# Performance work log

Measured on AMD Instinct MI355X. Metric: run time of the kernel, lower is better.

## Reference

```python
import jax, jax.numpy as jnp
import numpy as np

DIM = 256
NUM_HEADS = 8
HEAD_DIM = DIM // NUM_HEADS


def setup_inputs() -> dict:
    key = jax.random.key(0)
    k1, k2, k3, k4 = jax.random.split(key, 4)
    b, n = 4, 2048
    x = jax.random.normal(k1, (b, n, DIM), dtype=jnp.float32)
    # Linear weights with fan-in scaling (matches nn.Linear init magnitude,
    # keeps exp(qk) numerically sane since the original has no max-subtraction).
    Wqkv = jax.random.normal(k2, (DIM, 3 * DIM), dtype=jnp.float32) * (DIM ** -0.5)
    Wout = jax.random.normal(k3, (DIM, DIM), dtype=jnp.float32) * (DIM ** -0.5)
    bout = jax.random.normal(k4, (DIM,), dtype=jnp.float32) * 0.01
    return {"x": x, "Wqkv": Wqkv, "Wout": Wout, "bout": bout}


def reference(x, Wqkv, Wout, bout):
    b, n, d = x.shape
    h, hd = NUM_HEADS, HEAD_DIM
    scale = hd ** -0.5
    qkv = x @ Wqkv  # [b, n, 3d]
    q, k, v = jnp.split(qkv, 3, axis=-1)
    # [b, h, n, hd]
    q = q.reshape(b, n, h, hd).transpose(0, 2, 1, 3) * scale
    k = k.reshape(b, n, h, hd).transpose(0, 2, 1, 3)
    v = v.reshape(b, n, h, hd).transpose(0, 2, 1, 3)
    # Original KeOps path: unnormalized exp (no max-subtraction), separate
    # numerator / denominator reductions, eps in denominator.
    scores = jnp.einsum('bhnd,bhmd->bhnm', q, k)  # [b, h, n, n]
    e = jnp.exp(scores)
    denom = jnp.sum(e, axis=-1, keepdims=True)          # [b, h, n, 1]
    numer = jnp.einsum('bhnm,bhmd->bhnd', e, v)         # [b, h, n, hd]
    out = numer / (denom + 1e-6)
    out = out.transpose(0, 2, 1, 3).reshape(b, n, d)
    return out @ Wout + bout
```

## Files before the change

### kernel.cpp

```cpp
#include <hip/hip_runtime.h>

#define DIM 256
#define NHEADS 8
#define HDIM 32

typedef _Float16 half8_t __attribute__((ext_vector_type(8)));
typedef _Float16 half4_t __attribute__((ext_vector_type(4)));
typedef float float4_t __attribute__((ext_vector_type(4)));

__device__ __forceinline__ void gload_lds16(const void* g, void* l) {
    __builtin_amdgcn_global_load_lds((const __attribute__((address_space(1))) void*)g,
                                     (__attribute__((address_space(3))) void*)l,
                                     16, 0, 0);
}

__global__ __launch_bounds__(256) void prep(const float* __restrict__ x,
                                            const float* __restrict__ Wqkv,
                                            const float* __restrict__ Wout,
                                            _Float16* __restrict__ xh,
                                            _Float16* __restrict__ WqT,
                                            _Float16* __restrict__ WoT) {
    __shared__ float ts[32][33];
    const int bid = blockIdx.x, t = threadIdx.x;
    if (bid < 1024) {
        size_t idx = (size_t)bid * 2048 + (size_t)t * 8;
        float tmp[8];
        *reinterpret_cast<float4*>(tmp)     = *reinterpret_cast<const float4*>(x + idx);
        *reinterpret_cast<float4*>(tmp + 4) = *reinterpret_cast<const float4*>(x + idx + 4);
        half8_t h;
        #pragma unroll
        for (int j = 0; j < 8; ++j) h[j] = (_Float16)tmp[j];
        *reinterpret_cast<half8_t*>(xh + idx) = h;
    } else {
        const float* src; _Float16* dst; int K, N, kb, nb;
        if (bid < 1024 + 192) { int b2 = bid - 1024; src = Wqkv; dst = WqT; K = 256; N = 768; nb = b2 % 24; kb = b2 / 24; }
        else                  { int b3 = bid - 1216; src = Wout; dst = WoT; K = 256; N = 256; nb = b3 % 8;  kb = b3 / 8; }
        const int tx = t & 31, ty = t >> 5;
        #pragma unroll
        for (int i = 0; i < 4; ++i) {
            int k = kb * 32 + ty + i * 8;
            ts[ty + i * 8][tx] = src[(size_t)k * N + nb * 32 + tx];
        }
        __syncthreads();
        #pragma unroll
        for (int i = 0; i < 4; ++i) {
            int nl = ty + i * 8;
            dst[(size_t)(nb * 32 + nl) * K + kb * 32 + tx] = (_Float16)ts[tx][nl];
        }
    }
}

__global__ __launch_bounds__(256) void gemm_qkv(const _Float16* __restrict__ A,
                                                const _Float16* __restrict__ BT,
                                                _Float16* __restrict__ qh,
                                                _Float16* __restrict__ kpack,
                                                _Float16* __restrict__ vp) {
    __shared__ alignas(16) _Float16 As[64 * 32];
    __shared__ alignas(16) _Float16 Bs[128 * 32];
    const int t = threadIdx.x, lane = t & 63, wave = t >> 6;
    const int l16 = lane & 15, quad = lane >> 4;
    const int m0 = blockIdx.y * 64, n0 = blockIdx.x * 128;
    const int wr = (wave >> 1) * 32, wc = (wave & 1) * 64;
    const int K = 256;

    float4_t acc[2][4];
    #pragma unroll
    for (int i = 0; i < 2; ++i)
        #pragma unroll
        for (int j = 0; j < 4; ++j) acc[i][j] = (float4_t){0.f, 0.f, 0.f, 0.f};

    const int srow = lane >> 2;
    const int scol = (lane & 3) * 8;

    for (int k0 = 0; k0 < K; k0 += 32) {
        gload_lds16(A  + (size_t)(m0 + wave * 16 + srow) * K + k0 + scol, As + wave * 512);
        gload_lds16(BT + (size_t)(n0 + wave * 16 + srow) * K + k0 + scol, Bs + wave * 512);
        gload_lds16(BT + (size_t)(n0 + 64 + wave * 16 + srow) * K + k0 + scol, Bs + 2048 + wave * 512);
        __syncthreads();
        half8_t af[2], bf[4];
        #pragma unroll
        for (int i = 0; i < 2; ++i)
            af[i] = *reinterpret_cast<const half8_t*>(As + (wr + i * 16 + l16) * 32 + quad * 8);
        #pragma unroll
        for (int j = 0; j < 4; ++j)
            bf[j] = *reinterpret_cast<const half8_t*>(Bs + (wc + j * 16 + l16) * 32 + quad * 8);
        #pragma unroll
        for (int i = 0; i < 2; ++i)
            #pragma unroll
            for (int j = 0; j < 4; ++j)
                acc[i][j] = __builtin_amdgcn_mfma_f32_16x16x32_f16(af[i], bf[j], acc[i][j], 0, 0, 0);
        __syncthreads();
    }

    const int bb = m0 >> 11;
    if (n0 < 256) {
        #pragma unroll
        for (int i = 0; i < 2; ++i)
            #pragma unroll
            for (int r = 0; r < 4; ++r) {
                int row = m0 + wr + i * 16 + quad * 4 + r;
                #pragma unroll
                for (int j = 0; j < 4; ++j)
                    qh[(size_t)row * 256 + n0 + wc + j * 16 + l16] = (_Float16)acc[i][j][r];
            }
    } else if (n0 < 512) {
        #pragma unroll
        for (int i = 0; i < 2; ++i)
            #pragma unroll
            for (int r = 0; r < 4; ++r) {
                int tok = (m0 & 2047) + wr + i * 16 + quad * 4 + r;
                #pragma unroll
                for (int j = 0; j < 4; ++j) {
                    int kc = n0 + wc + j * 16 + l16 - 256;
                    int hh = kc >> 5, dd = kc & 31;
                    kpack[((size_t)(bb * NHEADS + hh) * 2048 + tok) * 32 + dd] =
                        (_Float16)acc[i][j][r];
                }
            }
    } else {
        #pragma unroll
        for (int i = 0; i < 2; ++i) {
            int tok0 = (m0 & 2047) + wr + i * 16 + quad * 4;
            int chunk = tok0 >> 5, tl = tok0 & 31;
            #pragma unroll
            for (int j = 0; j < 4; ++j) {
                int vc = n0 + wc + j * 16 + l16 - 512;
                int hh = vc >> 5, dd = vc & 31;
                half4_t p;
                #pragma unroll
                for (int r = 0; r < 4; ++r) p[r] = (_Float16)acc[i][j][r];
                *reinterpret_cast<half4_t*>(
                    vp + (((size_t)(bb * NHEADS + hh) * 64 + chunk) * 32 + dd) * 32 + tl) = p;
            }
        }
    }
}

__global__ __launch_bounds__(256, 2) void attn_v7(const _Float16* __restrict__ qh,
                                                  const _Float16* __restrict__ kpack,
                                                  const _Float16* __restrict__ vp,
                                                  _Float16* __restrict__ NUM,
                                                  float* __restrict__ DEN) {
    __shared__ alignas(16) _Float16 es[4][64][40];
    const int bid = blockIdx.x;
    const int kh = bid & 1;
    const int qb = (bid >> 1) & 7;
    const int bh = bid >> 4;
    const int b = bh >> 3, h = bh & 7;
    const int t = threadIdx.x, lane = t & 63, wave = t >> 6;
    const int l16 = lane & 15, quad = lane >> 4;
    const float scale = 0.17677669529663687f;
    const int bN = b * 2048;
    const int q0w = qb * 256 + wave * 64;
    const int kbeg = kh * 1024;

    half8_t qf[4];
    {
        const _Float16* qrow = qh + (size_t)(bN + q0w + l16) * 256 + h * HDIM + quad * 8;
        #pragma unroll
        for (int g = 0; g < 4; ++g)
            qf[g] = *reinterpret_cast<const half8_t*>(qrow + (size_t)g * 16 * 256);
    }

    const _Float16* kb_ = kpack + (size_t)bh * 65536;
    const _Float16* vb_ = vp + (size_t)bh * 65536;

    float4_t num[4][2];
    #pragma unroll
    for (int g = 0; g < 4; ++g)
        #pragma unroll
        for (int dt = 0; dt < 2; ++dt) num[g][dt] = (float4_t){0.f, 0.f, 0.f, 0.f};
    float ds[4] = {0.f, 0.f, 0.f, 0.f};
    _Float16* esw = &es[wave][0][0];
    const float4_t z = {0.f, 0.f, 0.f, 0.f};

    for (int k0 = kbeg; k0 < kbeg + 1024; k0 += 64) {
        half8_t kf[4], vf[4];
        #pragma unroll
        for (int j = 0; j < 4; ++j)
            kf[j] = *reinterpret_cast<const half8_t*>(
                kb_ + (size_t)(k0 + j * 16 + l16) * 32 + quad * 8);
        const int c0 = k0 >> 5;
        #pragma unroll
        for (int s = 0; s < 2; ++s)
            #pragma unroll
            for (int m = 0; m < 2; ++m)
                vf[s * 2 + m] = *reinterpret_cast<const half8_t*>(
                    vb_ + ((size_t)(c0 + s) * 32 + m * 16 + l16) * 32 + quad * 8);

        float4_t st[4][4];
        #pragma unroll
        for (int kb = 0; kb < 4; ++kb)
            #pragma unroll
            for (int g = 0; g < 4; ++g)
                st[kb][g] = __builtin_amdgcn_mfma_f32_16x16x32_f16(kf[kb], qf[g], z, 0, 0, 0);

        half4_t ep[4][4];
        #pragma unroll
        for (int kb = 0; kb < 4; ++kb)
            #pragma unroll
            for (int g = 0; g < 4; ++g)
                #pragma unroll
                for (int r = 0; r < 4; ++r) {
                    float e = __expf(st[kb][g][r] * scale);
                    ds[g] += e;
                    ep[kb][g][r] = (_Float16)e;
                }

        #pragma unroll
        for (int s = 0; s < 2; ++s) {
            #pragma unroll
            for (int tt = 0; tt < 2; ++tt)
                #pragma unroll
                for (int g = 0; g < 4; ++g)
                    *reinterpret_cast<half4_t*>(
                        esw + (g * 16 + l16) * 40 + tt * 16 + quad * 4) = ep[s * 2 + tt][g];

            #pragma unroll
            for (int g = 0; g < 4; ++g) {
                half8_t ef = *reinterpret_cast<const half8_t*>(
                    esw + (g * 16 + l16) * 40 + quad * 8);
                num[g][0] = __builtin_amdgcn_mfma_f32_16x16x32_f16(ef, vf[s * 2],     num[g][0], 0, 0, 0);
                num[g][1] = __builtin_amdgcn_mfma_f32_16x16x32_f16(ef, vf[s * 2 + 1], num[g][1], 0, 0, 0);
            }
        }
    }

    #pragma unroll
    for (int g = 0; g < 4; ++g) {
        ds[g] += __shfl_xor(ds[g], 16, 64);
        ds[g] += __shfl_xor(ds[g], 32, 64);
    }

    _Float16* ob = NUM + (size_t)kh * 2097152 + (size_t)(bN + q0w) * DIM + h * HDIM;
    #pragma unroll
    for (int g = 0; g < 4; ++g)
        #pragma unroll
        for (int r = 0; r < 4; ++r) {
            size_t ro = (size_t)(g * 16 + quad * 4 + r) * DIM;
            ob[ro + l16]      = (_Float16)num[g][0][r];
            ob[ro + 16 + l16] = (_Float16)num[g][1][r];
        }
    if (quad == 0) {
        #pragma unroll
        for (int g = 0; g < 4; ++g)
            DEN[kh * 65536 + bh * 2048 + q0w + g * 16 + l16] = ds[g];
    }
}

__global__ __launch_bounds__(256) void gemm2c(const _Float16* __restrict__ NUM,
                                              const float* __restrict__ DEN,
                                              const _Float16* __restrict__ BT,
                                              const float* __restrict__ bias,
                                              float* __restrict__ out) {
    __shared__ alignas(16) _Float16 As[64 * 32];
    __shared__ alignas(16) _Float16 Bs[64 * 32];
    const int t = threadIdx.x, lane = t & 63, wave = t >> 6;
    const int l16 = lane & 15, quad = lane >> 4;
    const int m0 = blockIdx.y * 64, n0 = blockIdx.x * 64;
    const int wr = (wave >> 1) * 32, wc = (wave & 1) * 32;
    const int bb = m0 >> 11;

    const int arow = t >> 2;
    const int acol = (t & 3) * 8;
    const int myrow = m0 + arow;
    _Float16 rcp8[8];
    #pragma unroll
    for (int hh = 0; hh < 8; ++hh) {
        int di = (bb * 8 + hh) * 2048 + (myrow & 2047);
        rcp8[hh] = (_Float16)(1.f / (DEN[di] + DEN[di + 65536] + 1e-6f));
    }
    const _Float16* np = NUM + (size_t)myrow * 256 + acol;

    float4_t acc[2][2];
    #pragma unroll
    for (int i = 0; i < 2; ++i)
        #pragma unroll
        for (int j = 0; j < 2; ++j) acc[i][j] = (float4_t){0.f, 0.f, 0.f, 0.f};

    for (int k0 = 0; k0 < 256; k0 += 32) {
        half8_t n0h = *reinterpret_cast<const half8_t*>(np + k0);
        half8_t n1h = *reinterpret_cast<const half8_t*>(np + k0 + 2097152);
        *reinterpret_cast<half8_t*>(As + arow * 32 + acol) = (n0h + n1h) * rcp8[k0 >> 5];
        gload_lds16(BT + (size_t)(n0 + arow) * 256 + k0 + acol, Bs + t * 8);
        __syncthreads();
        half8_t af[2], bf[2];
        #pragma unroll
        for (int i = 0; i < 2; ++i)
            af[i] = *reinterpret_cast<const half8_t*>(As + (wr + i * 16 + l16) * 32 + quad * 8);
        #pragma unroll
        for (int j = 0; j < 2; ++j)
            bf[j] = *reinterpret_cast<const half8_t*>(Bs + (wc + j * 16 + l16) * 32 + quad * 8);
        #pragma unroll
        for (int i = 0; i < 2; ++i)
            #pragma unroll
            for (int j = 0; j < 2; ++j)
                acc[i][j] = __builtin_amdgcn_mfma_f32_16x16x32_f16(af[i], bf[j], acc[i][j], 0, 0, 0);
        __syncthreads();
    }

    #pragma unroll
    for (int i = 0; i < 2; ++i)
        #pragma unroll
        for (int r = 0; r < 4; ++r) {
            int row = m0 + wr + i * 16 + quad * 4 + r;
            #pragma unroll
            for (int j = 0; j < 2; ++j) {
                int col = n0 + wc + j * 16 + l16;
                out[(size_t)row * 256 + col] = acc[i][j][r] + bias[col];
            }
        }
}

extern "C" void kernel_launch(void* const* d_in, const int* in_sizes, int n_in,
                              void* d_out, int out_size, void* d_ws, size_t ws_size,
                              hipStream_t stream) {
    const float* x    = (const float*)d_in[0];
    const float* Wqkv = (const float*)d_in[1];
    const float* Wout = (const float*)d_in[2];
    const float* bout = (const float*)d_in[3];
    float* out = (float*)d_out;
    const int M = 8192;

    _Float16* xh    = (_Float16*)d_ws;
    _Float16* WqT   = xh + (size_t)M * DIM;
    _Float16* WoT   = WqT + 768 * 256;
    _Float16* qh    = WoT + 256 * 256;
    _Float16* kpack = qh + (size_t)M * DIM;
    _Float16* vp    = kpack + (size_t)32 * 2048 * 32;
    _Float16* NUM   = vp + (size_t)32 * 2048 * 32;
    float*    DEN   = (float*)(NUM + (size_t)2 * M * DIM);

    hipLaunchKernelGGL(prep, dim3(1280), dim3(256), 0, stream, x, Wqkv, Wout, xh, WqT, WoT);
    hipLaunchKernelGGL(gemm_qkv, dim3(6, 128), dim3(256), 0, stream, xh, WqT, qh, kpack, vp);
    hipLaunchKernelGGL(attn_v7, dim3(512), dim3(256), 0, stream, qh, kpack, vp, NUM, DEN);
    hipLaunchKernelGGL(gemm2c, dim3(4, 128), dim3(256), 0, stream, NUM, DEN, WoT, bout, out);
}
```

Before: 126.0 us.

## Split attention keys four ways, fold scale into Q, use MFMA for row sums

The x-to-fp16 conversion moves out of the prep kernel and into the QKV GEMM's A-tile load, so the xh round trip through memory goes away. The softmax scale times log2(e) is folded into Q at GEMM time so attention can use exp2 directly. The attention denominator is now accumulated with an extra MFMA against a ones vector, replacing the scalar adds and shuffles. The key range is split four ways instead of two, doubling the block count with launch bounds of 4, at the cost of more partial NUM/DEN traffic that the output GEMM must sum.

```diff
diff --git a/kernel.cpp b/kernel.cpp
--- a/kernel.cpp
+++ b/kernel.cpp
@@ -14,43 +14,30 @@
                                      16, 0, 0);
 }
 
-__global__ __launch_bounds__(256) void prep(const float* __restrict__ x,
-                                            const float* __restrict__ Wqkv,
-                                            const float* __restrict__ Wout,
-                                            _Float16* __restrict__ xh,
-                                            _Float16* __restrict__ WqT,
-                                            _Float16* __restrict__ WoT) {
+#define QSCALE 0.25503093964976485f
+
+__global__ __launch_bounds__(256) void prep_w(const float* __restrict__ Wqkv,
+                                              const float* __restrict__ Wout,
+                                              _Float16* __restrict__ WqT,
+                                              _Float16* __restrict__ WoT) {
     __shared__ float ts[32][33];
     const int bid = blockIdx.x, t = threadIdx.x;
-    if (bid < 1024) {
-        size_t idx = (size_t)bid * 2048 + (size_t)t * 8;
-        float tmp[8];
-        *reinterpret_cast<float4*>(tmp)     = *reinterpret_cast<const float4*>(x + idx);
-        *reinterpret_cast<float4*>(tmp + 4) = *reinterpret_cast<const float4*>(x + idx + 4);
-        half8_t h;
-        #pragma unroll
-        for (int j = 0; j < 8; ++j) h[j] = (_Float16)tmp[j];
-        *reinterpret_cast<half8_t*>(xh + idx) = h;
-    } else {
-        const float* src; _Float16* dst; int K, N, kb, nb;
-        if (bid < 1024 + 192) { int b2 = bid - 1024; src = Wqkv; dst = WqT; K = 256; N = 768; nb = b2 % 24; kb = b2 / 24; }
-        else                  { int b3 = bid - 1216; src = Wout; dst = WoT; K = 256; N = 256; nb = b3 % 8;  kb = b3 / 8; }
-        const int tx = t & 31, ty = t >> 5;
-        #pragma unroll
-        for (int i = 0; i < 4; ++i) {
-            int k = kb * 32 + ty + i * 8;
-            ts[ty + i * 8][tx] = src[(size_t)k * N + nb * 32 + tx];
-        }
-        __syncthreads();
-        #pragma unroll
-        for (int i = 0; i < 4; ++i) {
-            int nl = ty + i * 8;
-            dst[(size_t)(nb * 32 + nl) * K + kb * 32 + tx] = (_Float16)ts[tx][nl];
-        }
-    }
-}
-
-__global__ __launch_bounds__(256) void gemm_qkv(const _Float16* __restrict__ A,
+    const float* src; _Float16* dst; int N, kb, nb;
+    if (bid < 192) { src = Wqkv; dst = WqT; N = 768; nb = bid % 24; kb = bid / 24; }
+    else           { int b3 = bid - 192; src = Wout; dst = WoT; N = 256; nb = b3 % 8; kb = b3 / 8; }
+    const int tx = t & 31, ty = t >> 5;
+    #pragma unroll
+    for (int i = 0; i < 4; ++i)
+        ts[ty + i * 8][tx] = src[(size_t)(kb * 32 + ty + i * 8) * N + nb * 32 + tx];
+    __syncthreads();
+    #pragma unroll
+    for (int i = 0; i < 4; ++i) {
+        int nl = ty + i * 8;
+        dst[(size_t)(nb * 32 + nl) * 256 + kb * 32 + tx] = (_Float16)ts[tx][nl];
+    }
+}
+
+__global__ __launch_bounds__(256) void gemm_qkv(const float* __restrict__ x,
                                                 const _Float16* __restrict__ BT,
                                                 _Float16* __restrict__ qh,
                                                 _Float16* __restrict__ kpack,
@@ -69,11 +56,22 @@
         #pragma unroll
         for (int j = 0; j < 4; ++j) acc[i][j] = (float4_t){0.f, 0.f, 0.f, 0.f};
 
+    const int arow = t >> 2;
+    const int acol = (t & 3) * 8;
     const int srow = lane >> 2;
     const int scol = (lane & 3) * 8;
 
     for (int k0 = 0; k0 < K; k0 += 32) {
-        gload_lds16(A  + (size_t)(m0 + wave * 16 + srow) * K + k0 + scol, As + wave * 512);
+        {
+            const float* xp = x + (size_t)(m0 + arow) * K + k0 + acol;
+            float tmp[8];
+            *reinterpret_cast<float4*>(tmp)     = *reinterpret_cast<const float4*>(xp);
+            *reinterpret_cast<float4*>(tmp + 4) = *reinterpret_cast<const float4*>(xp + 4);
+            half8_t h;
+            #pragma unroll
+            for (int j = 0; j < 8; ++j) h[j] = (_Float16)tmp[j];
+            *reinterpret_cast<half8_t*>(As + arow * 32 + acol) = h;
+        }
         gload_lds16(BT + (size_t)(n0 + wave * 16 + srow) * K + k0 + scol, Bs + wave * 512);
         gload_lds16(BT + (size_t)(n0 + 64 + wave * 16 + srow) * K + k0 + scol, Bs + 2048 + wave * 512);
         __syncthreads();
@@ -101,7 +99,8 @@
                 int row = m0 + wr + i * 16 + quad * 4 + r;
                 #pragma unroll
                 for (int j = 0; j < 4; ++j)
-                    qh[(size_t)row * 256 + n0 + wc + j * 16 + l16] = (_Float16)acc[i][j][r];
+                    qh[(size_t)row * 256 + n0 + wc + j * 16 + l16] =
+                        (_Float16)(acc[i][j][r] * QSCALE);
             }
     } else if (n0 < 512) {
         #pragma unroll
@@ -136,23 +135,22 @@
     }
 }
 
-__global__ __launch_bounds__(256, 2) void attn_v7(const _Float16* __restrict__ qh,
+__global__ __launch_bounds__(256, 4) void attn_v8(const _Float16* __restrict__ qh,
                                                   const _Float16* __restrict__ kpack,
                                                   const _Float16* __restrict__ vp,
                                                   _Float16* __restrict__ NUM,
                                                   float* __restrict__ DEN) {
     __shared__ alignas(16) _Float16 es[4][64][40];
     const int bid = blockIdx.x;
-    const int kh = bid & 1;
-    const int qb = (bid >> 1) & 7;
-    const int bh = bid >> 4;
+    const int kh = bid & 3;
+    const int qb = (bid >> 2) & 7;
+    const int bh = bid >> 5;
     const int b = bh >> 3, h = bh & 7;
     const int t = threadIdx.x, lane = t & 63, wave = t >> 6;
     const int l16 = lane & 15, quad = lane >> 4;
-    const float scale = 0.17677669529663687f;
     const int bN = b * 2048;
     const int q0w = qb * 256 + wave * 64;
-    const int kbeg = kh * 1024;
+    const int kbeg = kh * 512;
 
     half8_t qf[4];
     {
@@ -165,16 +163,22 @@
     const _Float16* kb_ = kpack + (size_t)bh * 65536;
     const _Float16* vb_ = vp + (size_t)bh * 65536;
 
-    float4_t num[4][2];
-    #pragma unroll
-    for (int g = 0; g < 4; ++g)
-        #pragma unroll
-        for (int dt = 0; dt < 2; ++dt) num[g][dt] = (float4_t){0.f, 0.f, 0.f, 0.f};
-    float ds[4] = {0.f, 0.f, 0.f, 0.f};
+    float4_t num[4][2], dacc[4];
+    #pragma unroll
+    for (int g = 0; g < 4; ++g) {
+        num[g][0] = (float4_t){0.f, 0.f, 0.f, 0.f};
+        num[g][1] = (float4_t){0.f, 0.f, 0.f, 0.f};
+        dacc[g]   = (float4_t){0.f, 0.f, 0.f, 0.f};
+    }
+    half8_t ones;
+    #pragma unroll
+    for (int j = 0; j < 8; ++j) ones[j] = (_Float16)1.0f;
+
     _Float16* esw = &es[wave][0][0];
     const float4_t z = {0.f, 0.f, 0.f, 0.f};
 
-    for (int k0 = kbeg; k0 < kbeg + 1024; k0 += 64) {
+    #pragma unroll 2
+    for (int k0 = kbeg; k0 < kbeg + 512; k0 += 64) {
         half8_t kf[4], vf[4];
         #pragma unroll
         for (int j = 0; j < 4; ++j)
@@ -201,11 +205,8 @@
             #pragma unroll
             for (int g = 0; g < 4; ++g)
                 #pragma unroll
-                for (int r = 0; r < 4; ++r) {
-                    float e = __expf(st[kb][g][r] * scale);
-                    ds[g] += e;
-                    ep[kb][g][r] = (_Float16)e;
-                }
+                for (int r = 0; r < 4; ++r)
+                    ep[kb][g][r] = (_Float16)__builtin_exp2f(st[kb][g][r]);
 
         #pragma unroll
         for (int s = 0; s < 2; ++s) {
@@ -222,14 +223,9 @@
                     esw + (g * 16 + l16) * 40 + quad * 8);
                 num[g][0] = __builtin_amdgcn_mfma_f32_16x16x32_f16(ef, vf[s * 2],     num[g][0], 0, 0, 0);
                 num[g][1] = __builtin_amdgcn_mfma_f32_16x16x32_f16(ef, vf[s * 2 + 1], num[g][1], 0, 0, 0);
-            }
-        }
-    }
-
-    #pragma unroll
-    for (int g = 0; g < 4; ++g) {
-        ds[g] += __shfl_xor(ds[g], 16, 64);
-        ds[g] += __shfl_xor(ds[g], 32, 64);
+                dacc[g]   = __builtin_amdgcn_mfma_f32_16x16x32_f16(ef, ones,          dacc[g],   0, 0, 0);
+            }
+        }
     }
 
     _Float16* ob = NUM + (size_t)kh * 2097152 + (size_t)(bN + q0w) * DIM + h * HDIM;
@@ -241,10 +237,12 @@
             ob[ro + l16]      = (_Float16)num[g][0][r];
             ob[ro + 16 + l16] = (_Float16)num[g][1][r];
         }
-    if (quad == 0) {
+    if (l16 == 0) {
         #pragma unroll
         for (int g = 0; g < 4; ++g)
-            DEN[kh * 65536 + bh * 2048 + q0w + g * 16 + l16] = ds[g];
+            #pragma unroll
+            for (int r = 0; r < 4; ++r)
+                DEN[kh * 65536 + bh * 2048 + q0w + g * 16 + quad * 4 + r] = dacc[g][r];
     }
 }
 
@@ -268,7 +266,8 @@
     #pragma unroll
     for (int hh = 0; hh < 8; ++hh) {
         int di = (bb * 8 + hh) * 2048 + (myrow & 2047);
-        rcp8[hh] = (_Float16)(1.f / (DEN[di] + DEN[di + 65536] + 1e-6f));
+        float d = DEN[di] + DEN[di + 65536] + DEN[di + 131072] + DEN[di + 196608];
+        rcp8[hh] = (_Float16)(1.f / (d + 1e-6f));
     }
     const _Float16* np = NUM + (size_t)myrow * 256 + acol;
 
@@ -279,9 +278,12 @@
         for (int j = 0; j < 2; ++j) acc[i][j] = (float4_t){0.f, 0.f, 0.f, 0.f};
 
     for (int k0 = 0; k0 < 256; k0 += 32) {
-        half8_t n0h = *reinterpret_cast<const half8_t*>(np + k0);
-        half8_t n1h = *reinterpret_cast<const half8_t*>(np + k0 + 2097152);
-        *reinterpret_cast<half8_t*>(As + arow * 32 + acol) = (n0h + n1h) * rcp8[k0 >> 5];
+        half8_t s0 = *reinterpret_cast<const half8_t*>(np + k0);
+        half8_t s1 = *reinterpret_cast<const half8_t*>(np + k0 + 2097152);
+        half8_t s2 = *reinterpret_cast<const half8_t*>(np + k0 + 2 * 2097152);
+        half8_t s3 = *reinterpret_cast<const half8_t*>(np + k0 + 3 * 2097152);
+        *reinterpret_cast<half8_t*>(As + arow * 32 + acol) =
+            ((s0 + s1) + (s2 + s3)) * rcp8[k0 >> 5];
         gload_lds16(BT + (size_t)(n0 + arow) * 256 + k0 + acol, Bs + t * 8);
         __syncthreads();
         half8_t af[2], bf[2];
@@ -322,17 +324,16 @@
     float* out = (float*)d_out;
     const int M = 8192;
 
-    _Float16* xh    = (_Float16*)d_ws;
-    _Float16* WqT   = xh + (size_t)M * DIM;
+    _Float16* WqT   = (_Float16*)d_ws;
     _Float16* WoT   = WqT + 768 * 256;
     _Float16* qh    = WoT + 256 * 256;
     _Float16* kpack = qh + (size_t)M * DIM;
     _Float16* vp    = kpack + (size_t)32 * 2048 * 32;
     _Float16* NUM   = vp + (size_t)32 * 2048 * 32;
-    float*    DEN   = (float*)(NUM + (size_t)2 * M * DIM);
-
-    hipLaunchKernelGGL(prep, dim3(1280), dim3(256), 0, stream, x, Wqkv, Wout, xh, WqT, WoT);
-    hipLaunchKernelGGL(gemm_qkv, dim3(6, 128), dim3(256), 0, stream, xh, WqT, qh, kpack, vp);
-    hipLaunchKernelGGL(attn_v7, dim3(512), dim3(256), 0, stream, qh, kpack, vp, NUM, DEN);
+    float*    DEN   = (float*)(NUM + (size_t)4 * M * DIM);
+
+    hipLaunchKernelGGL(prep_w, dim3(256), dim3(256), 0, stream, Wqkv, Wout, WqT, WoT);
+    hipLaunchKernelGGL(gemm_qkv, dim3(6, 128), dim3(256), 0, stream, x, WqT, qh, kpack, vp);
+    hipLaunchKernelGGL(attn_v8, dim3(1024), dim3(256), 0, stream, qh, kpack, vp, NUM, DEN);
     hipLaunchKernelGGL(gemm2c, dim3(4, 128), dim3(256), 0, stream, NUM, DEN, WoT, bout, out);
 }
```

Result: slower. 184.7 us (+46.6%).
